# Optimization experiments

Measured on AMD Instinct MI355X. Metric: run time of the kernel, lower is better.

The kernel has to match this reference:

```python
import jax, jax.numpy as jnp
import numpy as np

BATCH, SEQ, E, H = 8, 2048, 1024, 1024
LEAK = 0.95
SPECTRAL_RADIUS = 1.2
SPARSITY = 0.1


def setup_inputs() -> dict:
    rng = np.random.default_rng(0)
    x = rng.standard_normal((BATCH, SEQ, E)).astype(np.float32)
    # W_in: kaiming_uniform-like init
    bound = np.sqrt(1.0 / E)
    W_in = rng.uniform(-bound, bound, (H, E)).astype(np.float32)
    # W_res: sparse normal, rescaled to spectral radius 1.2
    W_res = rng.standard_normal((H, H)).astype(np.float32)
    mask = (rng.random((H, H)) > SPARSITY).astype(np.float32)
    W_res *= mask
    rad = np.max(np.abs(np.linalg.eigvals(W_res.astype(np.float64))))
    W_res = (W_res * (SPECTRAL_RADIUS / (rad + 1e-8))).astype(np.float32)
    s = 0.02
    inp = {
        "x": jnp.asarray(x),
        "W_in": jnp.asarray(W_in),
        "W_res": jnp.asarray(W_res),
        "norm_g": jnp.ones((E,), jnp.float32),
        "norm_b": jnp.zeros((E,), jnp.float32),
        "delta_w": jnp.asarray(rng.standard_normal((1, E)).astype(np.float32) * s),
        "delta_b": jnp.zeros((1,), jnp.float32),
        "A": jnp.full((H,), -10.0, jnp.float32),
        "B_w": jnp.asarray(rng.standard_normal((H, E)).astype(np.float32) * s),
        "ro_g": jnp.ones((H,), jnp.float32),
        "ro_b": jnp.zeros((H,), jnp.float32),
        "ro_w": jnp.asarray(rng.standard_normal((E, H)).astype(np.float32) * s),
        "ro_bias": jnp.zeros((E,), jnp.float32),
        "gate_w": jnp.asarray(rng.standard_normal((E, E)).astype(np.float32) * s),
        "gate_b": jnp.zeros((E,), jnp.float32),
    }
    return inp


def _layernorm(x, g, b, eps=1e-5):
    m = jnp.mean(x, axis=-1, keepdims=True)
    v = jnp.mean((x - m) ** 2, axis=-1, keepdims=True)
    return (x - m) * jax.lax.rsqrt(v + eps) * g + b


def reference(x, W_in, W_res, norm_g, norm_b, delta_w, delta_b, A, B_w,
              ro_g, ro_b, ro_w, ro_bias, gate_w, gate_b):
    x_norm = _layernorm(x, norm_g, norm_b)                      # [B,S,E]

    # --- TrueReservoir: leaky tanh RNN (scan over seq) ---
    xin = jnp.einsum('bse,he->bsh', x_norm, W_in)               # [B,S,H]
    h0 = jnp.zeros((x.shape[0], W_res.shape[0]), x.dtype)

    def res_step(h, u):
        new = jnp.tanh(u + h @ W_res.T)
        new = LEAK * new + (1.0 - LEAK) * h
        return new, new

    _, res_states = jax.lax.scan(res_step, h0, jnp.swapaxes(xin, 0, 1))
    res_states = jnp.swapaxes(res_states, 0, 1)                 # [B,S,H]

    ro_in = _layernorm(res_states, ro_g, ro_b)
    reservoir_out = jax.nn.gelu(jnp.einsum('bsh,eh->bse', ro_in, ro_w) + ro_bias,
                                approximate=False)              # [B,S,E]

    # --- selective SSM-style scan ---
    Bx = jnp.einsum('bse,he->bsh', x_norm, B_w)                 # [B,S,H]
    delta = jax.nn.softplus(jnp.einsum('bse,oe->bso', x_norm, delta_w) + delta_b)  # [B,S,1]
    A_bar = jnp.exp(A * delta)                                  # [B,S,H]
    B_bar = Bx * (1.0 - A_bar) / (A + 1e-8)                     # [B,S,H]

    def ssm_step(h, ab):
        a, b = ab
        h = a * h + b
        return h, h

    _, ssm_states = jax.lax.scan(
        ssm_step, h0, (jnp.swapaxes(A_bar, 0, 1), jnp.swapaxes(B_bar, 0, 1)))
    ssm_states = jnp.swapaxes(ssm_states, 0, 1)                 # [B,S,H]

    gate = jax.nn.sigmoid(jnp.einsum('bse,fe->bsf', x, gate_w) + gate_b)  # [B,S,E]
    return reservoir_out * gate + ssm_states * (1.0 - gate)
```

## Files before the change

kernel.cpp:

```cpp
#include <hip/hip_runtime.h>
#include <math.h>

#define B_ 8
#define S_ 2048
#define E_ 1024
#define H_ 1024
#define M_ 16384

typedef __attribute__((ext_vector_type(8))) short short8;
typedef __attribute__((ext_vector_type(4))) float floatx4;

__device__ __forceinline__ void block_reduce2(float &a, float &b) {
#pragma unroll
  for (int off = 32; off > 0; off >>= 1) {
    a += __shfl_down(a, off);
    b += __shfl_down(b, off);
  }
  __shared__ float sa[4], sb[4];
  const int w = threadIdx.x >> 6;
  __syncthreads();
  if ((threadIdx.x & 63) == 0) { sa[w] = a; sb[w] = b; }
  __syncthreads();
  a = sa[0] + sa[1] + sa[2] + sa[3];
  b = sb[0] + sb[1] + sb[2] + sb[3];
}

__device__ __forceinline__ unsigned pack_bf16(float lo, float hi) {
  return __builtin_amdgcn_perm(__float_as_uint(hi) + 0x8000u,
                               __float_as_uint(lo) + 0x8000u, 0x07060302u);
}
__device__ __forceinline__ unsigned pack_hi16(unsigned a, unsigned b) {
  return __builtin_amdgcn_perm(b, a, 0x07060302u);
}

__global__ __launch_bounds__(256) void ln_delta_kernel(
    const float* __restrict__ x, const float* __restrict__ g, const float* __restrict__ bt,
    const float* __restrict__ dw, const float* __restrict__ db,
    unsigned short* __restrict__ xnb, float* __restrict__ delta)
{
  const int row = blockIdx.x;
  const int t = threadIdx.x;
  const float4 v = ((const float4*)(x + (size_t)row * E_))[t];
  float s1 = v.x + v.y + v.z + v.w;
  float s2 = v.x*v.x + v.y*v.y + v.z*v.z + v.w*v.w;
  block_reduce2(s1, s2);
  const float mean = s1 * (1.f / E_);
  const float var  = s2 * (1.f / E_) - mean * mean;
  const float rstd = rsqrtf(var + 1e-5f);
  const float4 g4 = ((const float4*)g)[t];
  const float4 b4 = ((const float4*)bt)[t];
  float4 o;
  o.x = (v.x - mean) * rstd * g4.x + b4.x;
  o.y = (v.y - mean) * rstd * g4.y + b4.y;
  o.z = (v.z - mean) * rstd * g4.z + b4.z;
  o.w = (v.w - mean) * rstd * g4.w + b4.w;
  uint2 p;
  p.x = pack_bf16(o.x, o.y); p.y = pack_bf16(o.z, o.w);
  ((uint2*)(xnb + (size_t)row * E_))[t] = p;
  const float4 d4 = ((const float4*)dw)[t];
  float dd = o.x*d4.x + o.y*d4.y + o.z*d4.z + o.w*d4.w;
  float dummy = 0.f;
  block_reduce2(dd, dummy);
  if (t == 0) {
    const float z = dd + db[0];
    delta[row] = (z > 20.f) ? z : log1pf(__expf(z));
  }
}

__global__ __launch_bounds__(256) void rowstats_kernel(
    const float* __restrict__ res, float2* __restrict__ st)
{
  const int row = blockIdx.x;
  const int t = threadIdx.x;
  const float4 v = ((const float4*)(res + (size_t)row * H_))[t];
  float s1 = v.x + v.y + v.z + v.w;
  float s2 = v.x*v.x + v.y*v.y + v.z*v.z + v.w*v.w;
  block_reduce2(s1, s2);
  if (t == 0) {
    const float m = s1 * (1.f / H_);
    const float var = s2 * (1.f / H_) - m * m;
    st[row] = make_float2(m, rsqrtf(var + 1e-5f));
  }
}

__global__ __launch_bounds__(256) void tobf16_kernel(
    const float* __restrict__ s, unsigned short* __restrict__ d)
{
  const int i = blockIdx.x * 256 + threadIdx.x;
  const float4 v = ((const float4*)s)[i];
  uint2 p;
  p.x = pack_bf16(v.x, v.y); p.y = pack_bf16(v.z, v.w);
  ((uint2*)d)[i] = p;
}

__global__ __launch_bounds__(256) void splitw_kernel(
    const float* __restrict__ s, unsigned short* __restrict__ dh, unsigned short* __restrict__ dl)
{
  const int i = blockIdx.x * 256 + threadIdx.x;
  const float4 v = ((const float4*)s)[i];
  const float sv[4] = {v.x, v.y, v.z, v.w};
  unsigned h[4]; float l[4];
#pragma unroll
  for (int e = 0; e < 4; ++e) {
    h[e] = (__float_as_uint(sv[e]) + 0x8000u) & 0xFFFF0000u;
    l[e] = sv[e] - __uint_as_float(h[e]);
  }
  uint2 ph, pl;
  ph.x = pack_hi16(h[0], h[1]); ph.y = pack_hi16(h[2], h[3]);
  pl.x = pack_bf16(l[0], l[1]); pl.y = pack_bf16(l[2], l[3]);
  ((uint2*)dh)[i] = ph;
  ((uint2*)dl)[i] = pl;
}

__global__ __launch_bounds__(256) void gemm_bb(
    const unsigned short* __restrict__ A, const unsigned short* __restrict__ W,
    float* __restrict__ C)
{
  __shared__ __align__(16) unsigned short As[128 * 40];
  __shared__ __align__(16) unsigned short Ws[128 * 40];
  const int tid  = threadIdx.x;
  const int bn   = blockIdx.x & 7;
  const int bm   = blockIdx.x >> 3;
  const int wave = tid >> 6, lane = tid & 63;
  const int wm = (wave >> 1) * 64, wn = (wave & 1) * 64;
  const int fm = lane & 15, quad = lane >> 4;

  floatx4 acc[4][4];
#pragma unroll
  for (int i = 0; i < 4; ++i)
#pragma unroll
    for (int j = 0; j < 4; ++j) acc[i][j] = (floatx4){0.f, 0.f, 0.f, 0.f};

  const unsigned short* Abase = A + (size_t)bm * 128 * 1024;
  const unsigned short* Wbase = W + (size_t)bn * 128 * 1024;

  for (int k0 = 0; k0 < 1024; k0 += 32) {
    uint2 a2[4], w2[4];
#pragma unroll
    for (int i = 0; i < 4; ++i) {
      const int q = tid + 256 * i;
      const int row = q >> 3, ch = q & 7;
      a2[i] = *(const uint2*)(Abase + (size_t)row * 1024 + k0 + ch * 4);
      w2[i] = *(const uint2*)(Wbase + (size_t)row * 1024 + k0 + ch * 4);
    }
#pragma unroll
    for (int i = 0; i < 4; ++i) {
      const int q = tid + 256 * i;
      const int row = q >> 3, ch = q & 7;
      *(uint2*)(&As[row * 40 + ch * 4]) = a2[i];
      *(uint2*)(&Ws[row * 40 + ch * 4]) = w2[i];
    }
    __syncthreads();
    short8 af[4], wf[4];
#pragma unroll
    for (int i = 0; i < 4; ++i) {
      af[i] = *(const short8*)(&As[(wm + i * 16 + fm) * 40 + quad * 8]);
      wf[i] = *(const short8*)(&Ws[(wn + i * 16 + fm) * 40 + quad * 8]);
    }
#pragma unroll
    for (int i = 0; i < 4; ++i)
#pragma unroll
      for (int j = 0; j < 4; ++j)
        acc[i][j] = __builtin_amdgcn_mfma_f32_16x16x32_bf16(af[i], wf[j], acc[i][j], 0, 0, 0);
    __syncthreads();
  }

#pragma unroll
  for (int i = 0; i < 4; ++i) {
    const int grow0 = bm * 128 + wm + i * 16 + quad * 4;
#pragma unroll
    for (int j = 0; j < 4; ++j) {
      const int gcol = bn * 128 + wn + j * 16 + fm;
#pragma unroll
      for (int r = 0; r < 4; ++r)
        C[(size_t)(grow0 + r) * 1024 + gcol] = acc[i][j][r];
    }
  }
}

__global__ __launch_bounds__(256) void gemm_readout_mfma(
    const float* __restrict__ A,
    const unsigned short* __restrict__ Wh_g,
    const unsigned short* __restrict__ Wl_g,
    const float* __restrict__ bias,
    const float2* __restrict__ lnst,
    const float* __restrict__ lng, const float* __restrict__ lnb,
    const float* __restrict__ Avec,
    const float* __restrict__ cumd,
    const float* __restrict__ chH,
    const float* __restrict__ gate,
    float* __restrict__ C)
{
  __shared__ __align__(16) unsigned short Ah[128 * 40];
  __shared__ __align__(16) unsigned short Al[128 * 40];
  __shared__ __align__(16) unsigned short Wh[128 * 40];
  __shared__ __align__(16) unsigned short Wl[128 * 40];
  const int tid  = threadIdx.x;
  const int bn   = blockIdx.x & 7;
  const int bm   = blockIdx.x >> 3;
  const int wave = tid >> 6, lane = tid & 63;
  const int wm = (wave >> 1) * 64, wn = (wave & 1) * 64;
  const int fm = lane & 15, quad = lane >> 4;

  floatx4 acc[4][4];
#pragma unroll
  for (int i = 0; i < 4; ++i)
#pragma unroll
    for (int j = 0; j < 4; ++j) acc[i][j] = (floatx4){0.f, 0.f, 0.f, 0.f};

  const float* Abase = A + (size_t)bm * 128 * 1024;
  const unsigned short* Whb = Wh_g + (size_t)bn * 128 * 1024;
  const unsigned short* Wlb = Wl_g + (size_t)bn * 128 * 1024;

  float2 st_i[4];
#pragma unroll
  for (int i = 0; i < 4; ++i) {
    const int q = tid + 256 * i;
    st_i[i] = lnst[bm * 128 + (q >> 3)];
  }

  for (int k0 = 0; k0 < 1024; k0 += 32) {
#pragma unroll
    for (int i = 0; i < 4; ++i) {
      const int q = tid + 256 * i;
      const int row = q >> 3, ch = q & 7;
      float4 a4 = *(const float4*)(Abase + (size_t)row * 1024 + k0 + ch * 4);
      const float4 g4 = *(const float4*)(lng + k0 + ch * 4);
      const float4 b4 = *(const float4*)(lnb + k0 + ch * 4);
      const float2 st = st_i[i];
      a4.x = (a4.x - st.x) * st.y * g4.x + b4.x;
      a4.y = (a4.y - st.x) * st.y * g4.y + b4.y;
      a4.z = (a4.z - st.x) * st.y * g4.z + b4.z;
      a4.w = (a4.w - st.x) * st.y * g4.w + b4.w;
      const float av[4] = {a4.x, a4.y, a4.z, a4.w};
      unsigned ah[4]; float alr[4];
#pragma unroll
      for (int e = 0; e < 4; ++e) {
        ah[e] = (__float_as_uint(av[e]) + 0x8000u) & 0xFFFF0000u;
        alr[e] = av[e] - __uint_as_float(ah[e]);
      }
      uint2 pah, pal;
      pah.x = pack_hi16(ah[0], ah[1]); pah.y = pack_hi16(ah[2], ah[3]);
      pal.x = pack_bf16(alr[0], alr[1]); pal.y = pack_bf16(alr[2], alr[3]);
      *(uint2*)(&Ah[row * 40 + ch * 4]) = pah;
      *(uint2*)(&Al[row * 40 + ch * 4]) = pal;
      *(uint2*)(&Wh[row * 40 + ch * 4]) = *(const uint2*)(Whb + (size_t)row * 1024 + k0 + ch * 4);
      *(uint2*)(&Wl[row * 40 + ch * 4]) = *(const uint2*)(Wlb + (size_t)row * 1024 + k0 + ch * 4);
    }
    __syncthreads();
    short8 afh[4], afl[4], wfh[4], wfl[4];
#pragma unroll
    for (int i = 0; i < 4; ++i) {
      const int ao = (wm + i * 16 + fm) * 40 + quad * 8;
      const int wo = (wn + i * 16 + fm) * 40 + quad * 8;
      afh[i] = *(const short8*)(&Ah[ao]);
      afl[i] = *(const short8*)(&Al[ao]);
      wfh[i] = *(const short8*)(&Wh[wo]);
      wfl[i] = *(const short8*)(&Wl[wo]);
    }
#pragma unroll
    for (int i = 0; i < 4; ++i)
#pragma unroll
      for (int j = 0; j < 4; ++j) {
        acc[i][j] = __builtin_amdgcn_mfma_f32_16x16x32_bf16(afh[i], wfh[j], acc[i][j], 0, 0, 0);
        acc[i][j] = __builtin_amdgcn_mfma_f32_16x16x32_bf16(afl[i], wfh[j], acc[i][j], 0, 0, 0);
        acc[i][j] = __builtin_amdgcn_mfma_f32_16x16x32_bf16(afh[i], wfl[j], acc[i][j], 0, 0, 0);
      }
    __syncthreads();
  }

#pragma unroll
  for (int i = 0; i < 4; ++i) {
    const int grow0 = bm * 128 + wm + i * 16 + quad * 4;
    float cd_r[4];
    int hb_r[4];
#pragma unroll
    for (int r = 0; r < 4; ++r) {
      const int gr = grow0 + r;
      const int b = gr >> 11;
      const int c = (gr & 2047) >> 7;
      cd_r[r] = cumd[gr];
      hb_r[r] = (b * 16 + c) << 10;
    }
#pragma unroll
    for (int j = 0; j < 4; ++j) {
      const int gcol = bn * 128 + wn + j * 16 + fm;
      const float Ae = Avec[gcol];
      const float bb = bias[gcol];
#pragma unroll
      for (int r = 0; r < 4; ++r) {
        const int gr = grow0 + r;
        const size_t off = (size_t)gr * 1024 + gcol;
        const float hin = chH[hb_r[r] + gcol];
        const float lcl = C[off];
        const float gt  = gate[off];
        float v = acc[i][j][r] + bb;
        v = 0.5f * v * (1.f + erff(v * 0.70710678118654752f));
        const float p = __expf(Ae * cd_r[r]);
        const float sst = lcl + p * hin;
        C[off] = v * gt + sst * (1.f - gt);
      }
    }
  }
}

__global__ __launch_bounds__(512, 2) void scan_gate_kernel(
    float* __restrict__ xin_res,
    const float* __restrict__ Wres,
    unsigned* __restrict__ hbuf,
    const float* __restrict__ x,
    const float* __restrict__ gate_w,
    const float* __restrict__ gate_b,
    float* __restrict__ gateout)
{
  __shared__ __align__(16) unsigned char smem[20480];
  const int wg  = blockIdx.x;
  const int tid = threadIdx.x;

  if (wg < 128) {
    float* hsb = (float*)smem;
    const int go  = wg >> 4;
    const int mem = wg & 15;
    const int g   = tid >> 6;
    const int l   = tid & 63;
    const int row8 = mem * 64 + g * 8;

    float4 w4[8][4];
#pragma unroll
    for (int r = 0; r < 8; ++r) {
      const float* wrow = Wres + (size_t)(row8 + r) * 1024 + l * 16;
#pragma unroll
      for (int j = 0; j < 4; ++j) w4[r][j] = *(const float4*)(wrow + 4 * j);
    }

    const int m0 = l & 1, m1 = (l >> 1) & 1, m2 = (l >> 2) & 1;
    const int myrow = row8 + (l & 7);
    float hprev = 0.f;
    const unsigned long long tmask = 0x0000FFFF0000FFFFull;

    const int Pw = (tid >> 1) ^ ((tid >> 6) & 7);
    const int wofs = Pw * 4 + (tid & 1) * 2;

    for (int s = 0; s < S_; ++s) {
      const float u = xin_res[((size_t)go * S_ + s) * H_ + myrow];
      asm volatile("" :: "v"(u));

      const unsigned tag = (unsigned)s & 0xFFFFu;
      const unsigned long long tag2 = (unsigned long long)tag | ((unsigned long long)tag << 32);
      const unsigned long long* hp =
          (const unsigned long long*)(hbuf + (size_t)(s & 1) * 8192 + go * 1024) + tid;
      unsigned long long w;
      for (;;) {
        w = __hip_atomic_load(hp, __ATOMIC_RELAXED, __HIP_MEMORY_SCOPE_AGENT);
        if (((w ^ tag2) & tmask) == 0ull) break;
      }

      float2 hf;
      hf.x = __uint_as_float((unsigned)w & 0xFFFF0000u);
      hf.y = __uint_as_float((unsigned)(w >> 32) & 0xFFFF0000u);
      *(float2*)(hsb + (s & 1) * 1024 + wofs) = hf;
      __syncthreads();

      const float* hbse = hsb + (s & 1) * 1024;
      float acc0 = 0.f, acc1 = 0.f, acc2 = 0.f, acc3 = 0.f;
      float acc4 = 0.f, acc5 = 0.f, acc6 = 0.f, acc7 = 0.f;
#pragma unroll
      for (int j = 0; j < 4; ++j) {
        const int P = (4 * l + j) ^ ((l >> 3) & 7);
        const float4 h4 = *(const float4*)(hbse + P * 4);
        acc0 += w4[0][j].x * h4.x + w4[0][j].y * h4.y + w4[0][j].z * h4.z + w4[0][j].w * h4.w;
        acc1 += w4[1][j].x * h4.x + w4[1][j].y * h4.y + w4[1][j].z * h4.z + w4[1][j].w * h4.w;
        acc2 += w4[2][j].x * h4.x + w4[2][j].y * h4.y + w4[2][j].z * h4.z + w4[2][j].w * h4.w;
        acc3 += w4[3][j].x * h4.x + w4[3][j].y * h4.y + w4[3][j].z * h4.z + w4[3][j].w * h4.w;
        acc4 += w4[4][j].x * h4.x + w4[4][j].y * h4.y + w4[4][j].z * h4.z + w4[4][j].w * h4.w;
        acc5 += w4[5][j].x * h4.x + w4[5][j].y * h4.y + w4[5][j].z * h4.z + w4[5][j].w * h4.w;
        acc6 += w4[6][j].x * h4.x + w4[6][j].y * h4.y + w4[6][j].z * h4.z + w4[6][j].w * h4.w;
        acc7 += w4[7][j].x * h4.x + w4[7][j].y * h4.y + w4[7][j].z * h4.z + w4[7][j].w * h4.w;
      }

      float v0 = (m0 ? acc1 : acc0) + __shfl_xor(m0 ? acc0 : acc1, 1);
      float v1 = (m0 ? acc3 : acc2) + __shfl_xor(m0 ? acc2 : acc3, 1);
      float v2 = (m0 ? acc5 : acc4) + __shfl_xor(m0 ? acc4 : acc5, 1);
      float v3 = (m0 ? acc7 : acc6) + __shfl_xor(m0 ? acc6 : acc7, 1);
      float u0 = (m1 ? v1 : v0) + __shfl_xor(m1 ? v0 : v1, 2);
      float u1 = (m1 ? v3 : v2) + __shfl_xor(m1 ? v2 : v3, 2);
      float ps = (m2 ? u1 : u0) + __shfl_xor(m2 ? u0 : u1, 4);
      ps += __shfl_xor(ps, 8);
      ps += __shfl_xor(ps, 16);
      ps += __shfl_xor(ps, 32);

      const float z  = u + ps;
      const float e  = __expf(2.f * z);
      const float hn = 1.f - __fdividef(2.f, e + 1.f);
      const float hv = 0.95f * hn + 0.05f * hprev;
      hprev = hv;

      if (l < 8) {
        const unsigned word = ((__float_as_uint(hv) + 0x8000u) & 0xFFFF0000u)
                            | ((unsigned)(s + 1) & 0xFFFFu);
        __hip_atomic_store(hbuf + (size_t)((s + 1) & 1) * 8192 + go * 1024 + myrow, word,
                           __ATOMIC_RELAXED, __HIP_MEMORY_SCOPE_AGENT);
        xin_res[((size_t)go * S_ + s) * H_ + myrow] = hv;
      }
    }
  } else {
    unsigned short* As = (unsigned short*)smem;
    unsigned short* Ws = As + 128 * 40;
    const int bidx = wg - 128;
    const int bn   = bidx & 7;
    const int bm   = bidx >> 3;
    const bool act = tid < 256;
    const int wave = tid >> 6, lane = tid & 63;
    const int wm = (wave >> 1) * 64, wn = (wave & 1) * 64;
    const int fm = lane & 15, quad = lane >> 4;

    floatx4 acc[4][4];
#pragma unroll
    for (int i = 0; i < 4; ++i)
#pragma unroll
      for (int j = 0; j < 4; ++j) acc[i][j] = (floatx4){0.f, 0.f, 0.f, 0.f};

    const float* Abase = x + (size_t)bm * 128 * 1024;
    const float* Wbase = gate_w + (size_t)bn * 128 * 1024;

    for (int k0 = 0; k0 < 1024; k0 += 32) {
      if (act) {
        float4 a4[4], w4g[4];
#pragma unroll
        for (int i = 0; i < 4; ++i) {
          const int q = tid + 256 * i;
          const int row = q >> 3, ch = q & 7;
          a4[i]  = *(const float4*)(Abase + (size_t)row * 1024 + k0 + ch * 4);
          w4g[i] = *(const float4*)(Wbase + (size_t)row * 1024 + k0 + ch * 4);
        }
#pragma unroll
        for (int i = 0; i < 4; ++i) {
          const int q = tid + 256 * i;
          const int row = q >> 3, ch = q & 7;
          uint2 pa, pw;
          pa.x = pack_bf16(a4[i].x, a4[i].y);  pa.y = pack_bf16(a4[i].z, a4[i].w);
          pw.x = pack_bf16(w4g[i].x, w4g[i].y); pw.y = pack_bf16(w4g[i].z, w4g[i].w);
          *(uint2*)(&As[row * 40 + ch * 4]) = pa;
          *(uint2*)(&Ws[row * 40 + ch * 4]) = pw;
        }
      }
      __syncthreads();
      if (act) {
        short8 af[4], wf[4];
#pragma unroll
        for (int i = 0; i < 4; ++i) {
          af[i] = *(const short8*)(&As[(wm + i * 16 + fm) * 40 + quad * 8]);
          wf[i] = *(const short8*)(&Ws[(wn + i * 16 + fm) * 40 + quad * 8]);
        }
#pragma unroll
        for (int i = 0; i < 4; ++i)
#pragma unroll
          for (int j = 0; j < 4; ++j)
            acc[i][j] = __builtin_amdgcn_mfma_f32_16x16x32_bf16(af[i], wf[j], acc[i][j], 0, 0, 0);
      }
      __syncthreads();
    }

    if (act) {
#pragma unroll
      for (int i = 0; i < 4; ++i) {
        const int grow0 = bm * 128 + wm + i * 16 + quad * 4;
#pragma unroll
        for (int j = 0; j < 4; ++j) {
          const int gcol = bn * 128 + wn + j * 16 + fm;
          const float bb = gate_b[gcol];
#pragma unroll
          for (int r = 0; r < 4; ++r) {
            float v = acc[i][j][r] + bb;
            v = 1.f / (1.f + __expf(-v));
            gateout[(size_t)(grow0 + r) * 1024 + gcol] = v;
          }
        }
      }
    }
  }
}

__global__ __launch_bounds__(128) void cumd_kernel(
    const float* __restrict__ delta, float* __restrict__ cumd)
{
  const int t = threadIdx.x;
  const int b = t >> 4, c = t & 15;
  const int base = b * S_ + c * 128;
  float acc = 0.f;
  for (int i = 0; i < 128; ++i) { acc += delta[base + i]; cumd[base + i] = acc; }
}

__global__ __launch_bounds__(256) void ssm_partial_kernel(
    const float* __restrict__ delta, const float* __restrict__ Avec,
    float* __restrict__ bx, float* __restrict__ P)
{
  const int idx = blockIdx.x * 256 + threadIdx.x;
  const int h = idx & 1023;
  const int c = (idx >> 10) & 15;
  const int b = idx >> 14;
  const float Ah = Avec[h];
  const float inv = 1.f / (Ah + 1e-8f);
  const float* dp = delta + b * S_ + c * 128;
  float* xp = bx + ((size_t)(b * S_ + c * 128)) * H_ + h;
  float p = 1.f, hl = 0.f;
  for (int t = 0; t < 128; ++t) {
    const float a = __expf(Ah * dp[t]);
    const float bb = xp[(size_t)t * H_] * (1.f - a) * inv;
    hl = a * hl + bb;
    p *= a;
    xp[(size_t)t * H_] = hl;
  }
  P[(b * 16 + c) * 1024 + h] = p;
}

__global__ __launch_bounds__(256) void ssm_combine_kernel(
    const float* __restrict__ P, const float* __restrict__ local, float* __restrict__ Hin)
{
  const int idx = blockIdx.x * 256 + threadIdx.x;
  const int h = idx & 1023;
  const int b = idx >> 10;
  float hh = 0.f;
#pragma unroll
  for (int c = 0; c < 16; ++c) {
    const int o = (b * 16 + c) * 1024 + h;
    Hin[o] = hh;
    hh = P[o] * hh + local[((size_t)(b * S_ + c * 128 + 127)) * H_ + h];
  }
}

extern "C" void kernel_launch(void* const* d_in, const int* in_sizes, int n_in,
                              void* d_out, int out_size, void* d_ws, size_t ws_size,
                              hipStream_t stream) {
  (void)in_sizes; (void)n_in; (void)out_size; (void)ws_size;
  const float* x      = (const float*)d_in[0];
  const float* W_in   = (const float*)d_in[1];
  const float* W_res  = (const float*)d_in[2];
  const float* norm_g = (const float*)d_in[3];
  const float* norm_b = (const float*)d_in[4];
  const float* dw     = (const float*)d_in[5];
  const float* db     = (const float*)d_in[6];
  const float* Avec   = (const float*)d_in[7];
  const float* B_w    = (const float*)d_in[8];
  const float* ro_g   = (const float*)d_in[9];
  const float* ro_b   = (const float*)d_in[10];
  const float* ro_w   = (const float*)d_in[11];
  const float* ro_bias= (const float*)d_in[12];
  const float* gate_w = (const float*)d_in[13];
  const float* gate_b = (const float*)d_in[14];
  float* out = (float*)d_out;
  float* ws  = (float*)d_ws;

  float*    buf0   = ws;
  float*    buf1   = ws + 16777216;
  float*    delta  = ws + 33554432;
  float*    cumd   = ws + 33570816;
  unsigned* hbuf   = (unsigned*)(ws + 33587200);
  float2*   stats  = (float2*)(ws + 33603712);
  float*    chP    = ws + 33636480;
  float*    chH    = ws + 33767552;
  unsigned short* xnb = (unsigned short*)buf0;
  unsigned short* wib = (unsigned short*)(ws + 33898624);
  unsigned short* bwb = (unsigned short*)(ws + 34422912);
  unsigned short* roh = (unsigned short*)(ws + 34947200);
  unsigned short* rol = (unsigned short*)(ws + 35471488);

  tobf16_kernel<<<1024, 256, 0, stream>>>(W_in, wib);
  tobf16_kernel<<<1024, 256, 0, stream>>>(B_w, bwb);
  splitw_kernel<<<1024, 256, 0, stream>>>(ro_w, roh, rol);
  ln_delta_kernel<<<M_, 256, 0, stream>>>(x, norm_g, norm_b, dw, db, xnb, delta);
  gemm_bb<<<1024, 256, 0, stream>>>(xnb, wib, buf1);
  gemm_bb<<<1024, 256, 0, stream>>>(xnb, bwb, out);
  cumd_kernel<<<1, 128, 0, stream>>>(delta, cumd);
  ssm_partial_kernel<<<512, 256, 0, stream>>>(delta, Avec, out, chP);
  ssm_combine_kernel<<<32, 256, 0, stream>>>(chP, out, chH);
  hipMemsetAsync(hbuf, 0, 2 * 8192 * sizeof(unsigned), stream);
  scan_gate_kernel<<<1152, 512, 0, stream>>>(buf1, W_res, hbuf, x, gate_w, gate_b, buf0);
  rowstats_kernel<<<M_, 256, 0, stream>>>(buf1, stats);
  gemm_readout_mfma<<<1024, 256, 0, stream>>>(buf1, roh, rol, ro_bias, stats, ro_g, ro_b,
                                              Avec, cumd, chH, buf0, out);
}
```

Before: 3.848 ms.

## Fold SSM partial scan and delta cumsum into the reservoir scan kernel

```diff
diff --git a/kernel.cpp b/kernel.cpp
--- a/kernel.cpp
+++ b/kernel.cpp
@@ -311,7 +311,12 @@
     const float* __restrict__ x,
     const float* __restrict__ gate_w,
     const float* __restrict__ gate_b,
-    float* __restrict__ gateout)
+    float* __restrict__ gateout,
+    const float* __restrict__ delta,
+    const float* __restrict__ Avec,
+    float* __restrict__ bx,
+    float* __restrict__ chP,
+    float* __restrict__ cumd)
 {
   __shared__ __align__(16) unsigned char smem[20480];
   const int wg  = blockIdx.x;
@@ -319,8 +324,8 @@
 
   if (wg < 128) {
     float* hsb = (float*)smem;
-    const int go  = wg >> 4;
-    const int mem = wg & 15;
+    const int go  = wg & 7;
+    const int mem = wg >> 3;
     const int g   = tid >> 6;
     const int l   = tid & 63;
     const int row8 = mem * 64 + g * 8;
@@ -403,7 +408,7 @@
         xin_res[((size_t)go * S_ + s) * H_ + myrow] = hv;
       }
     }
-  } else {
+  } else if (wg < 1152) {
     unsigned short* As = (unsigned short*)smem;
     unsigned short* Ws = As + 128 * 40;
     const int bidx = wg - 128;
@@ -478,40 +483,32 @@
         }
       }
     }
-  }
-}
-
-__global__ __launch_bounds__(128) void cumd_kernel(
-    const float* __restrict__ delta, float* __restrict__ cumd)
-{
-  const int t = threadIdx.x;
-  const int b = t >> 4, c = t & 15;
-  const int base = b * S_ + c * 128;
-  float acc = 0.f;
-  for (int i = 0; i < 128; ++i) { acc += delta[base + i]; cumd[base + i] = acc; }
-}
-
-__global__ __launch_bounds__(256) void ssm_partial_kernel(
-    const float* __restrict__ delta, const float* __restrict__ Avec,
-    float* __restrict__ bx, float* __restrict__ P)
-{
-  const int idx = blockIdx.x * 256 + threadIdx.x;
-  const int h = idx & 1023;
-  const int c = (idx >> 10) & 15;
-  const int b = idx >> 14;
-  const float Ah = Avec[h];
-  const float inv = 1.f / (Ah + 1e-8f);
-  const float* dp = delta + b * S_ + c * 128;
-  float* xp = bx + ((size_t)(b * S_ + c * 128)) * H_ + h;
-  float p = 1.f, hl = 0.f;
-  for (int t = 0; t < 128; ++t) {
-    const float a = __expf(Ah * dp[t]);
-    const float bb = xp[(size_t)t * H_] * (1.f - a) * inv;
-    hl = a * hl + bb;
-    p *= a;
-    xp[(size_t)t * H_] = hl;
-  }
-  P[(b * 16 + c) * 1024 + h] = p;
+  } else if (wg < 1408) {
+    const int idx = (wg - 1152) * 512 + tid;
+    const int h = idx & 1023;
+    const int c = (idx >> 10) & 15;
+    const int b = idx >> 14;
+    const float Ah = Avec[h];
+    const float inv = 1.f / (Ah + 1e-8f);
+    const float* dp = delta + b * S_ + c * 128;
+    float* xp = bx + ((size_t)(b * S_ + c * 128)) * H_ + h;
+    float p = 1.f, hl = 0.f;
+    for (int t = 0; t < 128; ++t) {
+      const float a = __expf(Ah * dp[t]);
+      const float bb2 = xp[(size_t)t * H_] * (1.f - a) * inv;
+      hl = a * hl + bb2;
+      p *= a;
+      xp[(size_t)t * H_] = hl;
+    }
+    chP[(b * 16 + c) * 1024 + h] = p;
+  } else {
+    if (tid < 128) {
+      const int b = tid >> 4, c = tid & 15;
+      const int base = b * S_ + c * 128;
+      float acc = 0.f;
+      for (int i = 0; i < 128; ++i) { acc += delta[base + i]; cumd[base + i] = acc; }
+    }
+  }
 }
 
 __global__ __launch_bounds__(256) void ssm_combine_kernel(
@@ -571,11 +568,10 @@
   ln_delta_kernel<<<M_, 256, 0, stream>>>(x, norm_g, norm_b, dw, db, xnb, delta);
   gemm_bb<<<1024, 256, 0, stream>>>(xnb, wib, buf1);
   gemm_bb<<<1024, 256, 0, stream>>>(xnb, bwb, out);
-  cumd_kernel<<<1, 128, 0, stream>>>(delta, cumd);
-  ssm_partial_kernel<<<512, 256, 0, stream>>>(delta, Avec, out, chP);
+  hipMemsetAsync(hbuf, 0, 2 * 8192 * sizeof(unsigned), stream);
+  scan_gate_kernel<<<1409, 512, 0, stream>>>(buf1, W_res, hbuf, x, gate_w, gate_b, buf0,
+                                             delta, Avec, out, chP, cumd);
   ssm_combine_kernel<<<32, 256, 0, stream>>>(chP, out, chH);
-  hipMemsetAsync(hbuf, 0, 2 * 8192 * sizeof(unsigned), stream);
-  scan_gate_kernel<<<1152, 512, 0, stream>>>(buf1, W_res, hbuf, x, gate_w, gate_b, buf0);
   rowstats_kernel<<<M_, 256, 0, stream>>>(buf1, stats);
   gemm_readout_mfma<<<1024, 256, 0, stream>>>(buf1, roh, rol, ro_bias, stats, ro_g, ro_b,
                                               Avec, cumd, chH, buf0, out);
```

Result: faster. 3.442 ms (-10.6%).
